# Kernel tuning notes

Hardware: AMD Instinct MI355X
Metric: run time of the kernel (lower is better)

## Reference

```python
import jax, jax.numpy as jnp
import numpy as np

NBITS = 16  # posit word size passed to posit_forward
ES = 1      # posit exponent-field size (standard posit16 uses es=1)


def posit_quant(x, nbits=NBITS, es=ES):
    """Round-trip float -> posit(nbits, es) -> float, vectorized.

    Emulates posit quantization: regime length determines how many fraction
    bits remain, mantissa is rounded to that precision, magnitude clamped to
    [minpos, maxpos]. Straight-through estimator keeps gradients useful.
    """
    absx = jnp.abs(x)
    sign = jnp.sign(x)
    safe = jnp.maximum(absx, 1e-30)
    scale = jnp.floor(jnp.log2(safe))                 # binary exponent
    useed_log2 = float(2 ** es)
    regime = jnp.floor(scale / useed_log2)
    rlen = jnp.where(regime >= 0, regime + 2.0, 1.0 - regime)  # regime bits
    fbits = jnp.clip(nbits - 1 - es - rlen, 0.0, 28.0)          # fraction bits left
    pw = jnp.exp2(fbits)
    m = safe * jnp.exp2(-scale)                       # mantissa in [1, 2)
    mq = 1.0 + jnp.round((m - 1.0) * pw) / pw
    maxscale = float((nbits - 2) * (2 ** es))         # maxpos = 2^((n-2)*2^es)
    mag = jnp.clip(mq * jnp.exp2(scale), jnp.exp2(-maxscale), jnp.exp2(maxscale))
    q = jnp.where(absx == 0.0, 0.0, sign * mag)
    return x + jax.lax.stop_gradient(q - x)           # straight-through


def posit_linear(x, W, b):
    # posit_forward: quantize operands, GEMM, quantize the accumulated output
    xq = posit_quant(x)
    Wq = posit_quant(W)
    bq = posit_quant(b)
    return posit_quant(xq @ Wq.T + bq)


def setup_inputs() -> dict:
    key = jax.random.key(0)
    ks = jax.random.split(key, 7)

    def w(k, o, i):
        return jax.random.normal(k, (o, i), jnp.float32) * (1.0 / np.sqrt(i))

    return {
        "x": jax.random.normal(ks[0], (4096, 2048), jnp.float32),
        "W0": w(ks[1], 8192, 2048),
        "b0": jax.random.normal(ks[2], (8192,), jnp.float32) * 0.01,
        "W1": w(ks[3], 8192, 8192),
        "b1": jax.random.normal(ks[4], (8192,), jnp.float32) * 0.01,
        "W2": w(ks[5], 2048, 8192),
        "b2": jax.random.normal(ks[6], (2048,), jnp.float32) * 0.01,
    }


def reference(x, W0, b0, W1, b1, W2, b2):
    # layer 0: posit linear + relu (clamp(min=0))
    h = jax.nn.relu(posit_linear(x, W0, b0))
    # layer 1: posit linear + relu
    h = jax.nn.relu(posit_linear(h, W1, b1))
    # layer 2: posit linear, identity activation
    return posit_linear(h, W2, b2)
```

## Files before the change

### kernel.cpp

```cpp
#include <hip/hip_runtime.h>
#include <hip/hip_bf16.h>
#include <cstdint>
#include <cstddef>

using bf16 = __hip_bfloat16;
typedef __attribute__((ext_vector_type(8))) short short8;
typedef __attribute__((ext_vector_type(4))) float f32x4;

__device__ __forceinline__ float posit_quant_f32(float x) {
  float absx = fabsf(x);
  float safe = fmaxf(absx, 1e-30f);
  uint32_t bits = __float_as_uint(safe);
  int scale = (int)((bits >> 23) & 0xFFu) - 127;
  int regime = scale >> 1;
  int rlen = (regime >= 0) ? (regime + 2) : (1 - regime);
  int fbits = 14 - rlen;
  fbits = fbits < 0 ? 0 : fbits;
  float pw = (float)(1 << fbits);
  float m = __uint_as_float((bits & 0x007FFFFFu) | 0x3F800000u);
  float mq = rintf((m - 1.0f) * pw) * (1.0f / pw) + 1.0f;
  float mag = mq * __uint_as_float((uint32_t)(scale + 127) << 23);
  mag = fminf(fmaxf(mag, 0x1p-28f), 0x1p28f);
  return (absx == 0.0f) ? 0.0f : copysignf(mag, x);
}

__device__ __forceinline__ ushort4 pq_bf16x4(float4 v) {
  ushort4 o;
  o.x = __builtin_bit_cast(unsigned short, __float2bfloat16(posit_quant_f32(v.x)));
  o.y = __builtin_bit_cast(unsigned short, __float2bfloat16(posit_quant_f32(v.y)));
  o.z = __builtin_bit_cast(unsigned short, __float2bfloat16(posit_quant_f32(v.z)));
  o.w = __builtin_bit_cast(unsigned short, __float2bfloat16(posit_quant_f32(v.w)));
  return o;
}

__global__ void kquant_all(const float* __restrict__ s0, bf16* __restrict__ d0,
                           const float* __restrict__ s1, bf16* __restrict__ d1,
                           const float* __restrict__ s2, bf16* __restrict__ d2,
                           const float* __restrict__ s3, bf16* __restrict__ d3,
                           long c0, long c1, long c2, long c3) {
  long i = (long)blockIdx.x * blockDim.x + threadIdx.x;
  long stride = (long)gridDim.x * blockDim.x;
  for (; i < c3; i += stride) {
    const float* s; bf16* d; long j;
    if (i < c0)      { s = s0; d = d0; j = i; }
    else if (i < c1) { s = s1; d = d1; j = i - c0; }
    else if (i < c2) { s = s2; d = d2; j = i - c1; }
    else             { s = s3; d = d3; j = i - c2; }
    float4 v = ((const float4*)s)[j];
    ((ushort4*)d)[j] = pq_bf16x4(v);
  }
}

__global__ void kcombine(const float* __restrict__ p, const float* __restrict__ bias,
                         float* __restrict__ out, long n4, long halfn, int cmask) {
  long i = (long)blockIdx.x * blockDim.x + threadIdx.x;
  long stride = (long)gridDim.x * blockDim.x;
  for (; i < n4; i += stride) {
    float4 a = ((const float4*)p)[i];
    float4 b = ((const float4*)(p + halfn))[i];
    int c0 = (int)(i & cmask) * 4;
    float4 o;
    o.x = posit_quant_f32(a.x + b.x + posit_quant_f32(bias[c0 + 0]));
    o.y = posit_quant_f32(a.y + b.y + posit_quant_f32(bias[c0 + 1]));
    o.z = posit_quant_f32(a.z + b.z + posit_quant_f32(bias[c0 + 2]));
    o.w = posit_quant_f32(a.w + b.w + posit_quant_f32(bias[c0 + 3]));
    ((float4*)out)[i] = o;
  }
}

typedef __attribute__((address_space(1))) uint32_t gu32;
typedef __attribute__((address_space(3))) uint32_t lu32;

#define SBAR()  do { __builtin_amdgcn_sched_barrier(0); __builtin_amdgcn_s_barrier(); \
                     __builtin_amdgcn_sched_barrier(0); } while (0)
#define VMCNT(N) asm volatile("s_waitcnt vmcnt(" #N ")" ::: "memory")

#define AB0 0
#define AB1 32768
#define BB0 65536
#define BB1 98304

#define STG(SRC, KT, H, DST) do { \
    const char* _s = (SRC) + (long)((H) * 128) * Kb + (long)(KT) * 128; \
    char* _d = smem + (DST) + (H) * 16384 + wave * 1024; \
    __builtin_amdgcn_global_load_lds((const gu32*)_s, (lu32*)_d, 16, 0, 0); \
    __builtin_amdgcn_global_load_lds((const gu32*)(_s + 64 * Kb), (lu32*)(_d + 8192), 16, 0, 0); \
  } while (0)

#define LDA8(AOFF, FI, CK) (*(const short8*)(smem + (AOFF) + aRel + (FI) * 2048 + (CK)))
#define LDB8(BOFF, FJ, CK) (*(const short8*)(smem + (BOFF) + bRel + (FJ) * 2048 + (CK)))

#define PREF_ALO(BUF) do { _Pragma("unroll") \
    for (int f = 0; f < 4; ++f) { ar[f][0] = LDA8(BUF, f, ck0); ar[f][1] = LDA8(BUF, f, ck1); } \
  } while (0)
#define PREF_AHI(BUF) do { _Pragma("unroll") \
    for (int f = 0; f < 4; ++f) { ar[f][0] = LDA8(BUF, f + 4, ck0); ar[f][1] = LDA8(BUF, f + 4, ck1); } \
  } while (0)
#define PREF_B(BUF) do { _Pragma("unroll") \
    for (int f = 0; f < 4; ++f) { br[f][0] = LDB8(BUF, f, ck0); br[f][1] = LDB8(BUF, f, ck1); } \
  } while (0)

#define MQALL(ACC0) do { \
    _Pragma("unroll") \
    for (int fi = 0; fi < 4; ++fi) { \
      _Pragma("unroll") \
      for (int fj = 0; fj < 4; ++fj) { \
        acc[(ACC0) + fi][fj] = __builtin_amdgcn_mfma_f32_16x16x32_bf16( \
            ar[fi][0], br[fj][0], acc[(ACC0) + fi][fj], 0, 0, 0); \
        acc[(ACC0) + fi][fj] = __builtin_amdgcn_mfma_f32_16x16x32_bf16( \
            ar[fi][1], br[fj][1], acc[(ACC0) + fi][fj], 0, 0, 0); \
      } \
    } \
  } while (0)

template <int MODE>
__global__ __launch_bounds__(512, 2) void gemm256_posit(
    const bf16* __restrict__ A, const bf16* __restrict__ B,
    const float* __restrict__ bias, void* __restrict__ out,
    int M, int N, int Kfull, int Kloop, int nbt, int cpx) {
  __shared__ __align__(1024) char smem[131072];

  const int tid  = threadIdx.x;
  const int lane = tid & 63;
  const int wave = tid >> 6;
  const int wr = wave >> 2;
  const int wc = wave & 3;

  const int flat = blockIdx.x;
  const int wgid = (flat & 7) * cpx + (flat >> 3);
  const int split = wgid / nbt;
  const int t = wgid - split * nbt;
  const int nbx = N >> 8;
  const long brow0 = (long)(t / nbx) * 256;
  const long bcol0 = (long)(t % nbx) * 256;

  const long Kb = (long)Kfull * 2;
  const long splitoff = (long)split * Kloop * 2;

  const int srow = tid >> 3;
  const int scb  = ((tid & 7) * 16) ^ (((tid >> 3) & 7) << 4);
  const char* srcA = (const char*)A + (brow0 + srow) * Kb + scb + splitoff;
  const char* srcB = (const char*)B + (bcol0 + srow) * Kb + scb + splitoff;

  const int fr  = lane & 15;
  const int swz = (lane & 7) << 4;
  const int ck0 = (((lane >> 4) << 4)) ^ swz;
  const int ck1 = (64 + ((lane >> 4) << 4)) ^ swz;
  const int aRel = wr * 16384 + fr * 128;
  const int bRel = wc * 8192 + fr * 128;

  f32x4 acc[8][4] = {};
  short8 ar[4][2], br[4][2];

  const int nkt = Kloop >> 6;
  const int np  = nkt >> 1;

  STG(srcA, 0, 0, AB0); STG(srcA, 0, 1, AB0);
  STG(srcB, 0, 0, BB0); STG(srcB, 0, 1, BB0);

#pragma unroll 1
  for (int i = 0; i < np; ++i) {
    const int t1 = (2 * i + 1) & (nkt - 1);
    const int t2 = (2 * i + 2) & (nkt - 1);

    VMCNT(0);
    SBAR();
    STG(srcA, t1, 0, AB1); STG(srcA, t1, 1, AB1);
    PREF_B(BB0); PREF_ALO(AB0);
    __builtin_amdgcn_s_setprio(1); MQALL(0); __builtin_amdgcn_s_setprio(0);
    STG(srcB, t1, 0, BB1); STG(srcB, t1, 1, BB1);
    PREF_AHI(AB0);
    __builtin_amdgcn_s_setprio(1); MQALL(4); __builtin_amdgcn_s_setprio(0);

    VMCNT(0);
    SBAR();
    STG(srcA, t2, 0, AB0); STG(srcA, t2, 1, AB0);
    PREF_B(BB1); PREF_ALO(AB1);
    __builtin_amdgcn_s_setprio(1); MQALL(0); __builtin_amdgcn_s_setprio(0);
    STG(srcB, t2, 0, BB0); STG(srcB, t2, 1, BB0);
    PREF_AHI(AB1);
    __builtin_amdgcn_s_setprio(1); MQALL(4); __builtin_amdgcn_s_setprio(0);
  }
  asm volatile("s_waitcnt vmcnt(0) lgkmcnt(0)" ::: "memory");

  const int orow = (lane >> 4) * 4;
  const long row0 = brow0 + wr * 128;
  const long col0 = bcol0 + wc * 64;
  const long obase = (MODE == 2) ? (long)split * M * N : 0;
#pragma unroll
  for (int fj = 0; fj < 4; ++fj) {
    const long col = col0 + fj * 16 + fr;
    const float bv = (MODE == 2) ? 0.0f : posit_quant_f32(bias[col]);
#pragma unroll
    for (int fi = 0; fi < 8; ++fi) {
#pragma unroll
      for (int q = 0; q < 4; ++q) {
        float v = acc[fi][fj][q];
        if (MODE != 2) {
          v = posit_quant_f32(v + bv);
          if (MODE == 0) v = fmaxf(v, 0.0f);
        }
        const long idx = obase + (row0 + fi * 16 + orow + q) * (long)N + col;
        if (MODE == 0) ((bf16*)out)[idx] = __float2bfloat16(v);
        else           ((float*)out)[idx] = v;
      }
    }
  }
}

#define GBM 128
#define GBN 128
#define GBK 32

__device__ __forceinline__ void gload_lds16(const void* g, void* l) {
  __builtin_amdgcn_global_load_lds((const gu32*)g, (lu32*)l, 16, 0, 0);
}

template <bool RELU, bool OUTBF16>
__global__ __launch_bounds__(256, 2) void gemm_bt_posit(
    const bf16* __restrict__ A, const bf16* __restrict__ B,
    const float* __restrict__ bias, void* __restrict__ out,
    int M, int N, int K) {
  __shared__ __align__(1024) bf16 sA[GBM][GBK];
  __shared__ __align__(1024) bf16 sB[GBN][GBK];

  const int tid = threadIdx.x;
  const int lane = tid & 63;
  const int wave = tid >> 6;
  const int wr = wave >> 1;
  const int wc = wave & 1;
  const long brow0 = (long)blockIdx.y * GBM;
  const long bcol0 = (long)blockIdx.x * GBN;

  const int srow = lane >> 2;
  const int scol = (lane & 3) * 8;
  const int seg0 = wave * 2;

  const bf16* gA0 = A + (brow0 + seg0 * 16 + srow) * (long)K + scol;
  const bf16* gA1 = A + (brow0 + seg0 * 16 + 16 + srow) * (long)K + scol;
  const bf16* gB0 = B + (bcol0 + seg0 * 16 + srow) * (long)K + scol;
  const bf16* gB1 = B + (bcol0 + seg0 * 16 + 16 + srow) * (long)K + scol;
  bf16* lA0 = (bf16*)sA + seg0 * 512;
  bf16* lA1 = lA0 + 512;
  bf16* lB0 = (bf16*)sB + seg0 * 512;
  bf16* lB1 = lB0 + 512;

  f32x4 acc[4][4] = {};
  const int fr = lane & 15;
  const int fk = (lane >> 4) * 8;

  for (int kt = 0; kt < K; kt += GBK) {
    __syncthreads();
    gload_lds16(gA0 + kt, lA0);
    gload_lds16(gA1 + kt, lA1);
    gload_lds16(gB0 + kt, lB0);
    gload_lds16(gB1 + kt, lB1);
    __syncthreads();

    short8 af[4], bfv[4];
#pragma unroll
    for (int i = 0; i < 4; ++i) af[i] = *(const short8*)&sA[wr * 64 + i * 16 + fr][fk];
#pragma unroll
    for (int j = 0; j < 4; ++j) bfv[j] = *(const short8*)&sB[wc * 64 + j * 16 + fr][fk];
#pragma unroll
    for (int i = 0; i < 4; ++i)
#pragma unroll
      for (int j = 0; j < 4; ++j)
        acc[i][j] = __builtin_amdgcn_mfma_f32_16x16x32_bf16(af[i], bfv[j], acc[i][j], 0, 0, 0);
  }

  const int orow = (lane >> 4) * 4;
  const long row0 = brow0 + wr * 64;
  const long col0 = bcol0 + wc * 64;
#pragma unroll
  for (int j = 0; j < 4; ++j) {
    const long col = col0 + j * 16 + fr;
    const float bv = posit_quant_f32(bias[col]);
#pragma unroll
    for (int i = 0; i < 4; ++i) {
#pragma unroll
      for (int q = 0; q < 4; ++q) {
        float v = posit_quant_f32(acc[i][j][q] + bv);
        if (RELU) v = fmaxf(v, 0.0f);
        const long idx = (row0 + i * 16 + orow + q) * (long)N + col;
        if (OUTBF16) ((bf16*)out)[idx] = __float2bfloat16(v);
        else         ((float*)out)[idx] = v;
      }
    }
  }
}

extern "C" void kernel_launch(void* const* d_in, const int* in_sizes, int n_in,
                              void* d_out, int out_size, void* d_ws, size_t ws_size,
                              hipStream_t stream) {
  const float* x  = (const float*)d_in[0];
  const float* W0 = (const float*)d_in[1];
  const float* b0 = (const float*)d_in[2];
  const float* W1 = (const float*)d_in[3];
  const float* b1 = (const float*)d_in[4];
  const float* W2 = (const float*)d_in[5];
  const float* b2 = (const float*)d_in[6];

  const int M = 4096, D0 = 2048, D1 = 8192, D2 = 8192, DO = 2048;

  char* ws = (char*)d_ws;
  size_t off = 0;
  auto alloc = [&](size_t bytes) {
    char* p = ws + off;
    off += (bytes + 255) & ~(size_t)255;
    return p;
  };
  bf16* xq  = (bf16*)alloc((size_t)M * D0 * 2);
  bf16* W0q = (bf16*)alloc((size_t)D1 * D0 * 2);
  bf16* W1q = (bf16*)alloc((size_t)D2 * D1 * 2);
  bf16* W2q = (bf16*)alloc((size_t)DO * D2 * 2);
  bf16* h0  = (bf16*)alloc((size_t)M * D1 * 2);
  bf16* h1  = (bf16*)alloc((size_t)M * D2 * 2);
  float* part = (float*)alloc((size_t)2 * M * DO * 4);
  const bool splitk = (off <= ws_size);
  (void)in_sizes; (void)n_in; (void)out_size;

  {
    long q0 = (long)M * D0 / 4;
    long q1 = q0 + (long)D1 * D0 / 4;
    long q2 = q1 + (long)D2 * D1 / 4;
    long q3 = q2 + (long)DO * D2 / 4;
    kquant_all<<<2048, 256, 0, stream>>>(x, xq, W0, W0q, W1, W1q, W2, W2q,
                                         q0, q1, q2, q3);
  }

  {
    int nbt = (D1 / 256) * (M / 256), nwg = nbt;
    gemm256_posit<0><<<dim3(nwg), dim3(512), 0, stream>>>(
        xq, W0q, b0, h0, M, D1, D0, D0, nbt, nwg / 8);
  }
  {
    int nbt = (D2 / 256) * (M / 256), nwg = nbt;
    gemm256_posit<0><<<dim3(nwg), dim3(512), 0, stream>>>(
        h0, W1q, b1, h1, M, D2, D1, D1, nbt, nwg / 8);
  }
  if (splitk) {
    int nbt = (DO / 256) * (M / 256);
    int nwg = nbt * 2;
    gemm256_posit<2><<<dim3(nwg), dim3(512), 0, stream>>>(
        h1, W2q, nullptr, part, M, DO, D2, D2 / 2, nbt, nwg / 8);
    long n4 = (long)M * DO / 4;
    kcombine<<<2048, 256, 0, stream>>>(part, b2, (float*)d_out, n4,
                                       (long)M * DO, DO / 4 - 1);
  } else {
    gemm_bt_posit<false, false><<<dim3(DO / GBN, M / GBM), dim3(256), 0, stream>>>(
        h1, W2q, b2, (float*)d_out, M, DO, D2);
  }
}
```

Before: 892.9 us.

## Use 4-wave workgroups with 128x128 per-wave tiles and grouped tile ordering

Changes the 256x256 GEMM from 8 waves (each 128x64) to 4 waves (each 128x128), so every wave holds an 8x8 MFMA accumulator grid. Each A fragment loaded from LDS is then reused across twice as many B fragments. The global-to-LDS staging is rewritten as eight single loads per thread, and the setprio interleaving of staging with compute is removed. Tiles are now mapped to blocks in 4-column groups for L2 locality. This raises register pressure (launch_bounds 256,1) and lowers occupancy and latency hiding, and the tile mapping hardcodes 16 row tiles.

```diff
diff --git a/kernel.cpp b/kernel.cpp
--- a/kernel.cpp
+++ b/kernel.cpp
@@ -80,41 +80,43 @@
 #define BB0 65536
 #define BB1 98304
 
-#define STG(SRC, KT, H, DST) do { \
-    const char* _s = (SRC) + (long)((H) * 128) * Kb + (long)(KT) * 128; \
-    char* _d = smem + (DST) + (H) * 16384 + wave * 1024; \
+#define STGU(SRC, KT, U, DST) do { \
+    const char* _s = (SRC) + (long)((U) * 32) * Kb + (long)(KT) * 128; \
+    char* _d = smem + (DST) + (U) * 4096 + wave * 1024; \
     __builtin_amdgcn_global_load_lds((const gu32*)_s, (lu32*)_d, 16, 0, 0); \
-    __builtin_amdgcn_global_load_lds((const gu32*)(_s + 64 * Kb), (lu32*)(_d + 8192), 16, 0, 0); \
+  } while (0)
+
+#define STG8(SRC, KT, DST) do { \
+    STGU(SRC, KT, 0, DST); STGU(SRC, KT, 1, DST); STGU(SRC, KT, 2, DST); \
+    STGU(SRC, KT, 3, DST); STGU(SRC, KT, 4, DST); STGU(SRC, KT, 5, DST); \
+    STGU(SRC, KT, 6, DST); STGU(SRC, KT, 7, DST); \
   } while (0)
 
 #define LDA8(AOFF, FI, CK) (*(const short8*)(smem + (AOFF) + aRel + (FI) * 2048 + (CK)))
 #define LDB8(BOFF, FJ, CK) (*(const short8*)(smem + (BOFF) + bRel + (FJ) * 2048 + (CK)))
 
-#define PREF_ALO(BUF) do { _Pragma("unroll") \
-    for (int f = 0; f < 4; ++f) { ar[f][0] = LDA8(BUF, f, ck0); ar[f][1] = LDA8(BUF, f, ck1); } \
-  } while (0)
-#define PREF_AHI(BUF) do { _Pragma("unroll") \
-    for (int f = 0; f < 4; ++f) { ar[f][0] = LDA8(BUF, f + 4, ck0); ar[f][1] = LDA8(BUF, f + 4, ck1); } \
-  } while (0)
-#define PREF_B(BUF) do { _Pragma("unroll") \
-    for (int f = 0; f < 4; ++f) { br[f][0] = LDB8(BUF, f, ck0); br[f][1] = LDB8(BUF, f, ck1); } \
-  } while (0)
-
-#define MQALL(ACC0) do { \
+#define TILE_COMPUTE(ABx, BBx) do { \
     _Pragma("unroll") \
-    for (int fi = 0; fi < 4; ++fi) { \
+    for (int fi = 0; fi < 8; ++fi) { ar[fi][0] = LDA8(ABx, fi, ck0); ar[fi][1] = LDA8(ABx, fi, ck1); } \
+    _Pragma("unroll") \
+    for (int fjp = 0; fjp < 4; ++fjp) { \
+      br[0][0] = LDB8(BBx, 2 * fjp, ck0);     br[0][1] = LDB8(BBx, 2 * fjp, ck1); \
+      br[1][0] = LDB8(BBx, 2 * fjp + 1, ck0); br[1][1] = LDB8(BBx, 2 * fjp + 1, ck1); \
       _Pragma("unroll") \
-      for (int fj = 0; fj < 4; ++fj) { \
-        acc[(ACC0) + fi][fj] = __builtin_amdgcn_mfma_f32_16x16x32_bf16( \
-            ar[fi][0], br[fj][0], acc[(ACC0) + fi][fj], 0, 0, 0); \
-        acc[(ACC0) + fi][fj] = __builtin_amdgcn_mfma_f32_16x16x32_bf16( \
-            ar[fi][1], br[fj][1], acc[(ACC0) + fi][fj], 0, 0, 0); \
+      for (int fi = 0; fi < 8; ++fi) { \
+        _Pragma("unroll") \
+        for (int fj = 0; fj < 2; ++fj) { \
+          acc[fi][2 * fjp + fj] = __builtin_amdgcn_mfma_f32_16x16x32_bf16( \
+              ar[fi][0], br[fj][0], acc[fi][2 * fjp + fj], 0, 0, 0); \
+          acc[fi][2 * fjp + fj] = __builtin_amdgcn_mfma_f32_16x16x32_bf16( \
+              ar[fi][1], br[fj][1], acc[fi][2 * fjp + fj], 0, 0, 0); \
+        } \
       } \
     } \
   } while (0)
 
 template <int MODE>
-__global__ __launch_bounds__(512, 2) void gemm256_posit(
+__global__ __launch_bounds__(256, 1) void gemm256_posit(
     const bf16* __restrict__ A, const bf16* __restrict__ B,
     const float* __restrict__ bias, void* __restrict__ out,
     int M, int N, int Kfull, int Kloop, int nbt, int cpx) {
@@ -123,16 +125,17 @@
   const int tid  = threadIdx.x;
   const int lane = tid & 63;
   const int wave = tid >> 6;
-  const int wr = wave >> 2;
-  const int wc = wave & 3;
+  const int wr = wave >> 1;
+  const int wc = wave & 1;
 
   const int flat = blockIdx.x;
   const int wgid = (flat & 7) * cpx + (flat >> 3);
   const int split = wgid / nbt;
   const int t = wgid - split * nbt;
-  const int nbx = N >> 8;
-  const long brow0 = (long)(t / nbx) * 256;
-  const long bcol0 = (long)(t % nbx) * 256;
+  const int trow = (t & 63) >> 2;
+  const int tcol = ((t >> 6) << 2) | (t & 3);
+  const long brow0 = (long)trow * 256;
+  const long bcol0 = (long)tcol * 256;
 
   const long Kb = (long)Kfull * 2;
   const long splitoff = (long)split * Kloop * 2;
@@ -147,48 +150,39 @@
   const int ck0 = (((lane >> 4) << 4)) ^ swz;
   const int ck1 = (64 + ((lane >> 4) << 4)) ^ swz;
   const int aRel = wr * 16384 + fr * 128;
-  const int bRel = wc * 8192 + fr * 128;
-
-  f32x4 acc[8][4] = {};
-  short8 ar[4][2], br[4][2];
+  const int bRel = wc * 16384 + fr * 128;
+
+  f32x4 acc[8][8] = {};
+  short8 ar[8][2], br[2][2];
 
   const int nkt = Kloop >> 6;
   const int np  = nkt >> 1;
 
-  STG(srcA, 0, 0, AB0); STG(srcA, 0, 1, AB0);
-  STG(srcB, 0, 0, BB0); STG(srcB, 0, 1, BB0);
+  STG8(srcA, 0, AB0); STG8(srcB, 0, BB0);
 
 #pragma unroll 1
   for (int i = 0; i < np; ++i) {
-    const int t1 = (2 * i + 1) & (nkt - 1);
+    const int t1 = 2 * i + 1;
     const int t2 = (2 * i + 2) & (nkt - 1);
 
     VMCNT(0);
     SBAR();
-    STG(srcA, t1, 0, AB1); STG(srcA, t1, 1, AB1);
-    PREF_B(BB0); PREF_ALO(AB0);
-    __builtin_amdgcn_s_setprio(1); MQALL(0); __builtin_amdgcn_s_setprio(0);
-    STG(srcB, t1, 0, BB1); STG(srcB, t1, 1, BB1);
-    PREF_AHI(AB0);
-    __builtin_amdgcn_s_setprio(1); MQALL(4); __builtin_amdgcn_s_setprio(0);
+    STG8(srcA, t1, AB1); STG8(srcB, t1, BB1);
+    TILE_COMPUTE(AB0, BB0);
 
     VMCNT(0);
     SBAR();
-    STG(srcA, t2, 0, AB0); STG(srcA, t2, 1, AB0);
-    PREF_B(BB1); PREF_ALO(AB1);
-    __builtin_amdgcn_s_setprio(1); MQALL(0); __builtin_amdgcn_s_setprio(0);
-    STG(srcB, t2, 0, BB0); STG(srcB, t2, 1, BB0);
-    PREF_AHI(AB1);
-    __builtin_amdgcn_s_setprio(1); MQALL(4); __builtin_amdgcn_s_setprio(0);
+    STG8(srcA, t2, AB0); STG8(srcB, t2, BB0);
+    TILE_COMPUTE(AB1, BB1);
   }
   asm volatile("s_waitcnt vmcnt(0) lgkmcnt(0)" ::: "memory");
 
   const int orow = (lane >> 4) * 4;
   const long row0 = brow0 + wr * 128;
-  const long col0 = bcol0 + wc * 64;
+  const long col0 = bcol0 + wc * 128;
   const long obase = (MODE == 2) ? (long)split * M * N : 0;
 #pragma unroll
-  for (int fj = 0; fj < 4; ++fj) {
+  for (int fj = 0; fj < 8; ++fj) {
     const long col = col0 + fj * 16 + fr;
     const float bv = (MODE == 2) ? 0.0f : posit_quant_f32(bias[col]);
 #pragma unroll
@@ -331,18 +325,18 @@
 
   {
     int nbt = (D1 / 256) * (M / 256), nwg = nbt;
-    gemm256_posit<0><<<dim3(nwg), dim3(512), 0, stream>>>(
+    gemm256_posit<0><<<dim3(nwg), dim3(256), 0, stream>>>(
         xq, W0q, b0, h0, M, D1, D0, D0, nbt, nwg / 8);
   }
   {
     int nbt = (D2 / 256) * (M / 256), nwg = nbt;
-    gemm256_posit<0><<<dim3(nwg), dim3(512), 0, stream>>>(
+    gemm256_posit<0><<<dim3(nwg), dim3(256), 0, stream>>>(
         h0, W1q, b1, h1, M, D2, D1, D1, nbt, nwg / 8);
   }
   if (splitk) {
     int nbt = (DO / 256) * (M / 256);
     int nwg = nbt * 2;
-    gemm256_posit<2><<<dim3(nwg), dim3(512), 0, stream>>>(
+    gemm256_posit<2><<<dim3(nwg), dim3(256), 0, stream>>>(
         h1, W2q, nullptr, part, M, DO, D2, D2 / 2, nbt, nwg / 8);
     long n4 = (long)M * DO / 4;
     kcombine<<<2048, 256, 0, stream>>>(part, b2, (float*)d_out, n4,
```

After: 1.451 ms. 62.6% more time.
